# Optimization experiments

Measured on AMD Instinct MI355X. Metric: run time of the kernel, lower is better.

Reference implementation:

```python
import jax, jax.numpy as jnp
import numpy as np

B, N, K, F, OUT = 32, 2000, 32, 64, 128

def setup_inputs() -> dict:
    key = jax.random.key(0)
    k1, k2, k3, k4, k5 = jax.random.split(key, 5)
    x = jax.random.normal(k1, (B, N, F), dtype=jnp.float32)
    neighborhood = jax.random.randint(k2, (N, K), 0, N, dtype=jnp.int64)
    distances = jax.random.uniform(k3, (N, K), dtype=jnp.float32)
    # Linear(k*(F+1), OUT): torch default init scale ~ 1/sqrt(fan_in)
    fan_in = K * (F + 1)
    W = jax.random.normal(k4, (OUT, fan_in), dtype=jnp.float32) / np.sqrt(fan_in)
    b = jax.random.normal(k5, (OUT,), dtype=jnp.float32) / np.sqrt(fan_in)
    return {"x": x, "neighborhood": neighborhood, "distances": distances, "W": W, "b": b}

def reference(x, neighborhood, distances, W, b):
    batch, seq_len, feat = x.shape          # [B, N, F]
    k = neighborhood.shape[1]
    gathered = x[:, neighborhood, :]        # [B, N, K, F] gather over sequence dim
    d = jnp.broadcast_to(distances[None, :, :, None], (batch, seq_len, k, 1))
    h = jnp.concatenate([gathered, d], axis=-1)        # [B, N, K, F+1]
    h = h.reshape(batch, seq_len, k * (feat + 1))      # [B, N, K*(F+1)]
    out = jnp.einsum('bnf,of->bno', h, W) + b          # [B, N, OUT]
    return out
```

## Files before the change

### kernel.cpp

```cpp
#include <hip/hip_runtime.h>
#include <hip/hip_bf16.h>
#include <stdint.h>

typedef __attribute__((ext_vector_type(8)))  __bf16   bf16x8;
typedef __attribute__((ext_vector_type(16))) float    f32x16;
typedef __attribute__((ext_vector_type(8)))  float    f32x8;

#define NB   32
#define NN   2000
#define NK   32
#define NF   64
#define NOUT 128
#define NSTEP 130

#define GLOBAL_AS __attribute__((address_space(1)))
#define LDS_AS    __attribute__((address_space(3)))
#define SB() __builtin_amdgcn_sched_barrier(0)

__global__ void kprep(const float* __restrict__ x, const float* __restrict__ dist,
                      const float* __restrict__ W,
                      __bf16* __restrict__ xb2, __bf16* __restrict__ db,
                      __bf16* __restrict__ Wf) {
  const int t = threadIdx.x;
  if (blockIdx.x < NN) {
    __shared__ __bf16 sm[32 * 66];
    const int n = blockIdx.x;
    const int bb = t >> 3;
    const int f0 = (t & 7) << 3;
    const float* src = x + ((size_t)bb * NN + n) * NF + f0;
    f32x8 v = *(const f32x8*)src;
    bf16x8 r;
#pragma unroll
    for (int j = 0; j < 8; ++j) r[j] = (__bf16)v[j];
    *(bf16x8*)&sm[bb * 66 + f0] = r;
    __syncthreads();
    const int col = t & 31, half = (t >> 5) & 1, s = t >> 6;
    bf16x8 o = *(const bf16x8*)&sm[col * 66 + s * 16 + half * 8];
    *(bf16x8*)((char*)xb2 + ((size_t)n << 12) + t * 16) = o;
    if (t < NK) db[n * NK + t] = (__bf16)dist[n * NK + t];
  } else {
    const int kstep = blockIdx.x - NN;
    const int lane = t & 63;
    const int wv = t >> 6;
    const int o = wv * 32 + (lane & 31);
    const int kbase = kstep * 16 + (lane >> 5) * 8;
    bf16x8 r;
#pragma unroll
    for (int j = 0; j < 8; ++j) {
      const int kg = kbase + j;
      const int c = (kg < 2048) ? ((kg >> 6) * 65 + (kg & 63)) : ((kg - 2048) * 65 + 64);
      r[j] = (__bf16)W[(size_t)o * 2080 + c];
    }
    *(bf16x8*)(Wf + (((size_t)kstep * 256 + t) << 3)) = r;
  }
}

__global__ __launch_bounds__(128, 2) void kmain(
    const int* __restrict__ nbrs, const float* __restrict__ bias,
    const __bf16* __restrict__ xb2, const __bf16* __restrict__ Wf,
    const __bf16* __restrict__ db, float* __restrict__ out) {
  __shared__ __align__(16) char lds[3][2][4096];

  const int t    = threadIdx.x;
  const int lane = t & 63;
  const int ogp  = t >> 6;
  const int col  = lane & 31;
  const int half = lane >> 5;
  const int n0   = blockIdx.x * 2;

  f32x16 acc00 = {}, acc01 = {}, acc10 = {}, acc11 = {};

  int myidx = 0;
  if (lane < NK) myidx = nbrs[(n0 + ogp) * NK + lane];

  const char* wfb = (const char*)Wf + (ogp << 11) + lane * 16;

  auto stage = [&](int buf, int c) {
    const int nb = __builtin_amdgcn_readlane(myidx, c);
    const char* g = (const char*)xb2 + ((size_t)nb << 12) + lane * 16;
    char* l = &lds[buf][ogp][0];
#pragma unroll
    for (int q = 0; q < 4; ++q)
      __builtin_amdgcn_global_load_lds(
          (const GLOBAL_AS uint32_t*)(g + (q << 10)),
          (LDS_AS uint32_t*)(l + (q << 10)), 16, 0, 0);
  };

  auto loadB = [&](bf16x8* B, int c) {
    const char* base = wfb + ((size_t)c << 14);
#pragma unroll
    for (int s = 0; s < 4; ++s) {
      B[s * 2 + 0] = *(const bf16x8*)(base + (s << 12));
      B[s * 2 + 1] = *(const bf16x8*)(base + (s << 12) + 1024);
    }
  };

  auto compute = [&](int buf, const bf16x8* B) {
    __builtin_amdgcn_s_setprio(1);
#pragma unroll
    for (int s = 0; s < 4; ++s) {
      const char* lb = &lds[buf][0][0] + (s << 10) + lane * 16;
      bf16x8 a0 = *(const bf16x8*)(lb);
      bf16x8 a1 = *(const bf16x8*)(lb + 4096);
      acc00 = __builtin_amdgcn_mfma_f32_32x32x16_bf16(a0, B[s * 2 + 0], acc00, 0, 0, 0);
      acc01 = __builtin_amdgcn_mfma_f32_32x32x16_bf16(a0, B[s * 2 + 1], acc01, 0, 0, 0);
      acc10 = __builtin_amdgcn_mfma_f32_32x32x16_bf16(a1, B[s * 2 + 0], acc10, 0, 0, 0);
      acc11 = __builtin_amdgcn_mfma_f32_32x32x16_bf16(a1, B[s * 2 + 1], acc11, 0, 0, 0);
    }
    __builtin_amdgcn_s_setprio(0);
  };

  bf16x8 BA[8], BB[8];

  stage(0, 0); SB();
  loadB(BA, 0); SB();
  stage(1, 1); SB();

#define HALF(C, CBUF, SBUF, BC, BL)                         \
  loadB(BL, (C) + 1); SB();                                 \
  asm volatile("s_waitcnt vmcnt(12)" ::: "memory");         \
  __builtin_amdgcn_s_barrier(); SB();                       \
  stage(SBUF, (C) + 2); SB();                               \
  compute(CBUF, BC);

  for (int base = 0; base < 30; base += 6) {
    HALF(base + 0, 0, 2, BA, BB)
    HALF(base + 1, 1, 0, BB, BA)
    HALF(base + 2, 2, 1, BA, BB)
    HALF(base + 3, 0, 2, BB, BA)
    HALF(base + 4, 1, 0, BA, BB)
    HALF(base + 5, 2, 1, BB, BA)
  }
#undef HALF
  loadB(BB, 31); SB();
  asm volatile("s_waitcnt vmcnt(12)" ::: "memory");
  __builtin_amdgcn_s_barrier(); SB();
  compute(0, BA);
  asm volatile("s_waitcnt vmcnt(0)" ::: "memory");
  __builtin_amdgcn_s_barrier(); SB();
  compute(1, BB);

#pragma unroll
  for (int s = 0; s < 2; ++s) {
    const char* wt = wfb + ((size_t)(128 + s) << 12);
    bf16x8 b0 = *(const bf16x8*)(wt);
    bf16x8 b1 = *(const bf16x8*)(wt + 1024);
    const char* dbase = (const char*)db + (size_t)n0 * 64 + s * 32 + half * 16;
    bf16x8 d0 = *(const bf16x8*)(dbase);
    bf16x8 d1 = *(const bf16x8*)(dbase + 64);
    acc00 = __builtin_amdgcn_mfma_f32_32x32x16_bf16(d0, b0, acc00, 0, 0, 0);
    acc01 = __builtin_amdgcn_mfma_f32_32x32x16_bf16(d0, b1, acc01, 0, 0, 0);
    acc10 = __builtin_amdgcn_mfma_f32_32x32x16_bf16(d1, b0, acc10, 0, 0, 0);
    acc11 = __builtin_amdgcn_mfma_f32_32x32x16_bf16(d1, b1, acc11, 0, 0, 0);
  }

  const int o0 = (ogp << 6) + col;
  const float bv0 = bias[o0], bv1 = bias[o0 + 32];
#pragma unroll
  for (int r = 0; r < 16; ++r) {
    const int row = (r & 3) + 8 * (r >> 2) + 4 * half;
    float* op = out + ((size_t)row * NN + n0) * NOUT + o0;
    op[0]         = acc00[r] + bv0;
    op[32]        = acc01[r] + bv1;
    op[NOUT]      = acc10[r] + bv0;
    op[NOUT + 32] = acc11[r] + bv1;
  }
}

extern "C" void kernel_launch(void* const* d_in, const int* in_sizes, int n_in,
                              void* d_out, int out_size, void* d_ws, size_t ws_size,
                              hipStream_t stream) {
  const float* x    = (const float*)d_in[0];
  const int*   nbrs = (const int*)d_in[1];
  const float* dist = (const float*)d_in[2];
  const float* W    = (const float*)d_in[3];
  const float* bias = (const float*)d_in[4];
  float* out = (float*)d_out;

  char* ws = (char*)d_ws;
  __bf16* xb2 = (__bf16*)(ws);
  __bf16* Wf  = (__bf16*)(ws + 8192000);
  __bf16* db  = (__bf16*)(ws + 8192000 + 532480);

  kprep<<<NN + NSTEP, 256, 0, stream>>>(x, dist, W, xb2, db, Wf);
  kmain<<<NN / 2, 128, 0, stream>>>(nbrs, bias, xb2, Wf, db, out);
}
```

Baseline: 60.50 us.

## Process four nodes per block with four waves and double-buffered two-neighbor stages

Each block now handles four output nodes with four waves (two node pairs by two output groups), and each pipeline step stages two neighbors at once into a double buffer instead of one neighbor into a triple buffer. Every wave loads twice as many weight fragments per step (16 vectors), which halves the number of barrier and wait periods and lets the block's two node pairs share staging work. In exchange it uses more registers (BA/BB grow to 16 each), more LDS (64 KB per block) and a shallower prefetch depth, so occupancy and latency hiding could drop.

```diff
diff --git a/kernel.cpp b/kernel.cpp
--- a/kernel.cpp
+++ b/kernel.cpp
@@ -55,86 +55,93 @@
   }
 }
 
-__global__ __launch_bounds__(128, 2) void kmain(
+__global__ __launch_bounds__(256, 2) void kmain(
     const int* __restrict__ nbrs, const float* __restrict__ bias,
     const __bf16* __restrict__ xb2, const __bf16* __restrict__ Wf,
     const __bf16* __restrict__ db, float* __restrict__ out) {
-  __shared__ __align__(16) char lds[3][2][4096];
+  __shared__ __align__(16) char lds[2][8][4096];
 
   const int t    = threadIdx.x;
   const int lane = t & 63;
-  const int ogp  = t >> 6;
+  const int w    = t >> 6;
+  const int nh   = w >> 1;
+  const int ogp  = w & 1;
   const int col  = lane & 31;
   const int half = lane >> 5;
-  const int n0   = blockIdx.x * 2;
+  const int n0   = blockIdx.x * 4;
+  const int q    = nh * 2 + ogp;
 
   f32x16 acc00 = {}, acc01 = {}, acc10 = {}, acc11 = {};
 
   int myidx = 0;
-  if (lane < NK) myidx = nbrs[(n0 + ogp) * NK + lane];
+  if (lane < NK) myidx = nbrs[(n0 + q) * NK + lane];
 
   const char* wfb = (const char*)Wf + (ogp << 11) + lane * 16;
 
-  auto stage = [&](int buf, int c) {
-    const int nb = __builtin_amdgcn_readlane(myidx, c);
-    const char* g = (const char*)xb2 + ((size_t)nb << 12) + lane * 16;
-    char* l = &lds[buf][ogp][0];
+  auto stage = [&](int buf, int sc) {
 #pragma unroll
-    for (int q = 0; q < 4; ++q)
-      __builtin_amdgcn_global_load_lds(
-          (const GLOBAL_AS uint32_t*)(g + (q << 10)),
-          (LDS_AS uint32_t*)(l + (q << 10)), 16, 0, 0);
+    for (int p = 0; p < 2; ++p) {
+      const int nb = __builtin_amdgcn_readlane(myidx, sc * 2 + p);
+      const char* g = (const char*)xb2 + ((size_t)nb << 12) + lane * 16;
+      char* l = &lds[buf][q * 2 + p][0];
+#pragma unroll
+      for (int qq = 0; qq < 4; ++qq)
+        __builtin_amdgcn_global_load_lds(
+            (const GLOBAL_AS uint32_t*)(g + (qq << 10)),
+            (LDS_AS uint32_t*)(l + (qq << 10)), 16, 0, 0);
+    }
   };
 
-  auto loadB = [&](bf16x8* B, int c) {
-    const char* base = wfb + ((size_t)c << 14);
+  auto loadB = [&](bf16x8* B, int sc) {
+    const char* base = wfb + ((size_t)sc << 15);
 #pragma unroll
-    for (int s = 0; s < 4; ++s) {
-      B[s * 2 + 0] = *(const bf16x8*)(base + (s << 12));
-      B[s * 2 + 1] = *(const bf16x8*)(base + (s << 12) + 1024);
+    for (int ps = 0; ps < 8; ++ps) {
+      B[ps * 2 + 0] = *(const bf16x8*)(base + (ps << 12));
+      B[ps * 2 + 1] = *(const bf16x8*)(base + (ps << 12) + 1024);
     }
   };
 
   auto compute = [&](int buf, const bf16x8* B) {
     __builtin_amdgcn_s_setprio(1);
 #pragma unroll
-    for (int s = 0; s < 4; ++s) {
-      const char* lb = &lds[buf][0][0] + (s << 10) + lane * 16;
-      bf16x8 a0 = *(const bf16x8*)(lb);
-      bf16x8 a1 = *(const bf16x8*)(lb + 4096);
-      acc00 = __builtin_amdgcn_mfma_f32_32x32x16_bf16(a0, B[s * 2 + 0], acc00, 0, 0, 0);
-      acc01 = __builtin_amdgcn_mfma_f32_32x32x16_bf16(a0, B[s * 2 + 1], acc01, 0, 0, 0);
-      acc10 = __builtin_amdgcn_mfma_f32_32x32x16_bf16(a1, B[s * 2 + 0], acc10, 0, 0, 0);
-      acc11 = __builtin_amdgcn_mfma_f32_32x32x16_bf16(a1, B[s * 2 + 1], acc11, 0, 0, 0);
+    for (int p = 0; p < 2; ++p) {
+#pragma unroll
+      for (int s = 0; s < 4; ++s) {
+        const char* la = &lds[buf][(nh * 2 + 0) * 2 + p][0] + (s << 10) + lane * 16;
+        const char* lb = &lds[buf][(nh * 2 + 1) * 2 + p][0] + (s << 10) + lane * 16;
+        bf16x8 a0 = *(const bf16x8*)(la);
+        bf16x8 a1 = *(const bf16x8*)(lb);
+        const int ps = p * 4 + s;
+        acc00 = __builtin_amdgcn_mfma_f32_32x32x16_bf16(a0, B[ps * 2 + 0], acc00, 0, 0, 0);
+        acc01 = __builtin_amdgcn_mfma_f32_32x32x16_bf16(a0, B[ps * 2 + 1], acc01, 0, 0, 0);
+        acc10 = __builtin_amdgcn_mfma_f32_32x32x16_bf16(a1, B[ps * 2 + 0], acc10, 0, 0, 0);
+        acc11 = __builtin_amdgcn_mfma_f32_32x32x16_bf16(a1, B[ps * 2 + 1], acc11, 0, 0, 0);
+      }
     }
     __builtin_amdgcn_s_setprio(0);
   };
 
-  bf16x8 BA[8], BB[8];
+  bf16x8 BA[16], BB[16];
 
   stage(0, 0); SB();
   loadB(BA, 0); SB();
-  stage(1, 1); SB();
 
-#define HALF(C, CBUF, SBUF, BC, BL)                         \
-  loadB(BL, (C) + 1); SB();                                 \
-  asm volatile("s_waitcnt vmcnt(12)" ::: "memory");         \
-  __builtin_amdgcn_s_barrier(); SB();                       \
-  stage(SBUF, (C) + 2); SB();                               \
-  compute(CBUF, BC);
+#define PERIOD(SC, BC, BL)                                   \
+  loadB(BL, (SC) + 1); SB();                                 \
+  asm volatile("s_waitcnt vmcnt(16)" ::: "memory");          \
+  __builtin_amdgcn_s_barrier(); SB();                        \
+  stage(((SC) + 1) & 1, (SC) + 1); SB();                     \
+  compute((SC) & 1, BC);
 
-  for (int base = 0; base < 30; base += 6) {
-    HALF(base + 0, 0, 2, BA, BB)
-    HALF(base + 1, 1, 0, BB, BA)
-    HALF(base + 2, 2, 1, BA, BB)
-    HALF(base + 3, 0, 2, BB, BA)
-    HALF(base + 4, 1, 0, BA, BB)
-    HALF(base + 5, 2, 1, BB, BA)
+  for (int sc = 0; sc < 14; sc += 2) {
+    PERIOD(sc + 0, BA, BB)
+    PERIOD(sc + 1, BB, BA)
   }
-#undef HALF
-  loadB(BB, 31); SB();
-  asm volatile("s_waitcnt vmcnt(12)" ::: "memory");
+#undef PERIOD
+  loadB(BB, 15); SB();
+  asm volatile("s_waitcnt vmcnt(16)" ::: "memory");
   __builtin_amdgcn_s_barrier(); SB();
+  stage(1, 15); SB();
   compute(0, BA);
   asm volatile("s_waitcnt vmcnt(0)" ::: "memory");
   __builtin_amdgcn_s_barrier(); SB();
@@ -145,7 +152,7 @@
     const char* wt = wfb + ((size_t)(128 + s) << 12);
     bf16x8 b0 = *(const bf16x8*)(wt);
     bf16x8 b1 = *(const bf16x8*)(wt + 1024);
-    const char* dbase = (const char*)db + (size_t)n0 * 64 + s * 32 + half * 16;
+    const char* dbase = (const char*)db + (size_t)(n0 + nh * 2) * 64 + s * 32 + half * 16;
     bf16x8 d0 = *(const bf16x8*)(dbase);
     bf16x8 d1 = *(const bf16x8*)(dbase + 64);
     acc00 = __builtin_amdgcn_mfma_f32_32x32x16_bf16(d0, b0, acc00, 0, 0, 0);
@@ -155,11 +162,12 @@
   }
 
   const int o0 = (ogp << 6) + col;
+  const int nn = n0 + nh * 2;
   const float bv0 = bias[o0], bv1 = bias[o0 + 32];
 #pragma unroll
   for (int r = 0; r < 16; ++r) {
     const int row = (r & 3) + 8 * (r >> 2) + 4 * half;
-    float* op = out + ((size_t)row * NN + n0) * NOUT + o0;
+    float* op = out + ((size_t)row * NN + nn) * NOUT + o0;
     op[0]         = acc00[r] + bv0;
     op[32]        = acc01[r] + bv1;
     op[NOUT]      = acc10[r] + bv0;
@@ -183,5 +191,5 @@
   __bf16* db  = (__bf16*)(ws + 8192000 + 532480);
 
   kprep<<<NN + NSTEP, 256, 0, stream>>>(x, dist, W, xb2, db, Wf);
-  kmain<<<NN / 2, 128, 0, stream>>>(nbrs, bias, xb2, Wf, db, out);
+  kmain<<<NN / 4, 256, 0, stream>>>(nbrs, bias, xb2, Wf, db, out);
 }
```

Result: faster. 58.83 us (-2.8%).
